# Optimization experiments

Measured on AMD Instinct MI355X. Metric: run time of the kernel, lower is better.

The kernel has to match this reference:

```python
import jax, jax.numpy as jnp
import numpy as np

NPOINT = 2048  # N // stride


def sqdist(a, b):
    # a: [B,M,3], b: [B,N,3] -> squared euclidean distances [B,M,N] (== cdist(...)**2)
    return (jnp.sum(a * a, -1)[:, :, None] + jnp.sum(b * b, -1)[:, None, :]
            - 2.0 * jnp.einsum('bmc,bnc->bmn', a, b))


def farthest_point_sample(xyz, npoint):
    # xyz [B,N,3] -> int32 [B,npoint]; deterministic start at point 0
    B, N, _ = xyz.shape

    def step(carry, _):
        distance, farthest = carry
        centroid = jnp.take_along_axis(xyz, farthest[:, None, None], axis=1)  # [B,1,3]
        d = jnp.sum((xyz - centroid) ** 2, -1)                                # [B,N]
        distance = jnp.minimum(distance, d)
        nxt = jnp.argmax(distance, -1).astype(jnp.int32)
        return (distance, nxt), farthest

    init = (jnp.full((B, N), 1e10, xyz.dtype), jnp.zeros((B,), jnp.int32))
    _, idx = jax.lax.scan(step, init, None, length=npoint)
    return idx.T  # [B, npoint]


def ball_query(radius, k, xyz, new_xyz):
    # faithful to torch ball_query: mask out-of-radius as N, sort indices, take first k,
    # replace padding with the first valid neighbor
    B, N, _ = xyz.shape
    sqd = sqdist(new_xyz, xyz)                                   # [B,S,N]
    gi = jnp.where(sqd > radius ** 2, N, jnp.arange(N, dtype=jnp.int32))
    gi = jnp.sort(gi, axis=-1)[:, :, :k]                         # [B,S,k]
    first = gi[:, :, :1]
    return jnp.where(gi == N, first, gi)


def three_interpolation(points, features, query):
    # points [B,S,3], features [B,D,S], query [B,N,3] -> [B,D,N]
    d = sqdist(query, points)                                    # [B,N,S]
    neg, idx = jax.lax.top_k(-d, 3)                              # 3 smallest dists
    w = 1.0 / (-neg + 1e-8)
    w = w / jnp.sum(w, -1, keepdims=True)                        # [B,N,3]
    g = jnp.take_along_axis(features[:, :, None, :], idx[:, None, :, :], axis=3)  # [B,D,N,3]
    return jnp.sum(g * w[:, None, :, :], -1)


def setup_inputs() -> dict:
    key = jax.random.key(0)
    k1, k2, k3, k4 = jax.random.split(key, 4)
    xyz = jax.random.uniform(k1, (4, 8192, 3), dtype=jnp.float32)
    features = jax.random.normal(k2, (4, 64, 8192), dtype=jnp.float32)
    W1 = jax.random.normal(k3, (128, 67), dtype=jnp.float32) * 0.05   # (3+64)->128 pointwise conv
    W2 = jax.random.normal(k4, (128, 192), dtype=jnp.float32) * 0.05  # (64+128)->128 pointwise conv
    return {"xyz": xyz, "features": features, "W1": W1, "W2": W2}


def reference(xyz, features, W1, W2):
    RADIUS, K = 0.2, 16
    # --- set abstraction (SABlock): FPS -> ball query -> group -> conv -> maxpool ---
    sidx = farthest_point_sample(xyz, NPOINT)                        # [B,S]
    new_xyz = jnp.take_along_axis(xyz, sidx[:, :, None], axis=1)     # [B,S,3]
    nidx = ball_query(RADIUS, K, xyz, new_xyz)                       # [B,S,K]
    gxyz = jnp.take_along_axis(xyz[:, None, :, :], nidx[:, :, :, None], axis=2)  # [B,S,K,3]
    rel = gxyz - new_xyz[:, :, None, :]                              # relative coords
    gfeat = jnp.take_along_axis(features[:, :, None, :], nidx[:, None, :, :], axis=3)  # [B,D,S,K]
    grouped = jnp.concatenate([rel.transpose(0, 3, 1, 2), gfeat], axis=1)  # [B,3+D,S,K]
    h = jax.nn.relu(jnp.einsum('od,bdsk->bosk', W1, grouped))
    sub_x = jnp.max(h, -1)                                           # [B,O,S]
    # --- feature propagation (UpBlock): 3-NN interpolation back to N -> concat -> conv ---
    lerp = three_interpolation(new_xyz, sub_x, xyz)                  # [B,O,N]
    cat = jnp.concatenate([features, lerp], axis=1)                  # [B,D+O,N]
    return jax.nn.relu(jnp.einsum('od,bdn->bon', W2, cat))           # [B,O,N]
```

## Files before the change

### kernel.cpp

```cpp
#include <hip/hip_runtime.h>
#include <hip/hip_bf16.h>

#define BATCH 4
#define NPTS  8192
#define NSAMP 2048
#define NK    16
#define CFEAT 64
#define CG    67
#define CO1   128
#define CCAT  192
#define CO2   128

#define DEV __device__ __forceinline__

typedef float f32x2 __attribute__((ext_vector_type(2)));

DEV float n3(float x, float y, float z) {
    return __fadd_rn(__fadd_rn(__fmul_rn(x, x), __fmul_rn(y, y)), __fmul_rn(z, z));
}
DEV float dot3(float ax, float ay, float az, float bx, float by, float bz) {
    return __fmaf_rn(az, bz, __fmaf_rn(ay, by, __fmul_rn(ax, bx)));
}
DEV float sqd_expand(float an, float bn, float d) {
    return __fsub_rn(__fadd_rn(an, bn), __fmul_rn(2.0f, d));
}

DEV f32x2 pk_add(f32x2 a, f32x2 b) {
    f32x2 d;
    asm("v_pk_add_f32 %0, %1, %2" : "=v"(d) : "v"(a), "v"(b));
    return d;
}
DEV f32x2 pk_mul(f32x2 a, f32x2 b) {
    f32x2 d;
    asm("v_pk_mul_f32 %0, %1, %2" : "=v"(d) : "v"(a), "v"(b));
    return d;
}

#define DPPMAX(x, ctrl)                                                        \
    x = fmaxf(x, __int_as_float(__builtin_amdgcn_update_dpp(                   \
            __float_as_int(x), __float_as_int(x), (ctrl), 0xF, 0xF, false)))

template <int CTRL>
DEV void dpp_shr_max64(unsigned& hi, unsigned& lo) {
    unsigned nh = (unsigned)__builtin_amdgcn_update_dpp((int)hi, (int)hi, CTRL, 0xF, 0xF, false);
    unsigned nl = (unsigned)__builtin_amdgcn_update_dpp((int)lo, (int)lo, CTRL, 0xF, 0xF, false);
    unsigned long long a = ((unsigned long long)hi << 32) | lo;
    unsigned long long n = ((unsigned long long)nh << 32) | nl;
    if (n > a) { hi = nh; lo = nl; }
}

DEV float rlane(float v, int l) {
    return __int_as_float(__builtin_amdgcn_readlane(__float_as_int(v), l));
}

__global__ __launch_bounds__(256) void transpose_kernel(const float* __restrict__ F,
                                                        float* __restrict__ T) {
    __shared__ float tile[64][65];
    const int b = blockIdx.y;
    const int n0 = blockIdx.x * 64;
    const int tx = threadIdx.x & 63, ty = threadIdx.x >> 6;
    const float* Fb = F + (size_t)b * CFEAT * NPTS;
    float* Tb = T + (size_t)b * NPTS * CFEAT;
#pragma unroll
    for (int i = 0; i < 16; i++) {
        int c = ty + i * 4;
        tile[c][tx] = Fb[(size_t)c * NPTS + n0 + tx];
    }
    __syncthreads();
#pragma unroll
    for (int i = 0; i < 16; i++) {
        int r = ty + i * 4;
        Tb[(size_t)(n0 + r) * CFEAT + tx] = tile[tx][r];
    }
}

__global__ __launch_bounds__(512, 2) void fps_kernel(const float* __restrict__ xyz,
                                                     float* __restrict__ new_xyz) {
    const int b = blockIdx.x;
    const int t = threadIdx.x;
    const int lane = t & 63, wv = t >> 6;
    const float* X = xyz + (size_t)b * NPTS * 3;

    __shared__ f32x2 sxy[NPTS];
    __shared__ float szl[NPTS];
    __shared__ unsigned long long wred[2][8];

    f32x2 px[8], py[8], pz[8], dd[8];
    {
        const float4* X4 = (const float4*)X;
#pragma unroll
        for (int g = 0; g < 4; g++) {
            float4 f0 = X4[t * 12 + g * 3 + 0];
            float4 f1 = X4[t * 12 + g * 3 + 1];
            float4 f2 = X4[t * 12 + g * 3 + 2];
            px[2*g+0].x = f0.x; py[2*g+0].x = f0.y; pz[2*g+0].x = f0.z;
            px[2*g+0].y = f0.w; py[2*g+0].y = f1.x; pz[2*g+0].y = f1.y;
            px[2*g+1].x = f1.z; py[2*g+1].x = f1.w; pz[2*g+1].x = f2.x;
            px[2*g+1].y = f2.y; py[2*g+1].y = f2.z; pz[2*g+1].y = f2.w;
        }
#pragma unroll
        for (int j = 0; j < 8; j++) {
            int p = t * 16 + 2 * j;
            sxy[p].x = px[j].x; sxy[p].y = py[j].x; szl[p] = pz[j].x;
            sxy[p+1].x = px[j].y; sxy[p+1].y = py[j].y; szl[p+1] = pz[j].y;
            dd[j].x = 1e10f; dd[j].y = 1e10f;
        }
    }
    __syncthreads();

    f32x2 c0 = sxy[0];
    float cx = c0.x, cy = c0.y, cz = szl[0];
    if (t == 0) {
        size_t o = (size_t)b * NSAMP * 3;
        new_xyz[o + 0] = cx; new_xyz[o + 1] = cy; new_xyz[o + 2] = cz;
    }

    int par = 0;
    for (int s = 1; s < NSAMP; s++) {
        const float ncx = -cx, ncy = -cy, ncz = -cz;
        const f32x2 vcx = {ncx, ncx}, vcy = {ncy, ncy}, vcz = {ncz, ncz};
#pragma unroll
        for (int j = 0; j < 8; j++) {
            f32x2 dx = pk_add(px[j], vcx);
            f32x2 dy = pk_add(py[j], vcy);
            f32x2 dz = pk_add(pz[j], vcz);
            f32x2 d = pk_add(pk_add(pk_mul(dx, dx), pk_mul(dy, dy)), pk_mul(dz, dz));
            dd[j].x = fminf(dd[j].x, d.x);
            dd[j].y = fminf(dd[j].y, d.y);
        }
        float m[8];
#pragma unroll
        for (int j = 0; j < 8; j++) m[j] = fmaxf(dd[j].x, dd[j].y);
#pragma unroll
        for (int j = 0; j < 4; j++) m[j] = fmaxf(m[j], m[j + 4]);
        float bv = fmaxf(fmaxf(m[0], m[1]), fmaxf(m[2], m[3]));
        int bj = 15;
#pragma unroll
        for (int j = 14; j >= 0; --j) {
            float dj = (j & 1) ? dd[j >> 1].y : dd[j >> 1].x;
            if (dj == bv) bj = j;
        }
        const int lidx = t * 16 + bj;

        float wm = bv;
        DPPMAX(wm, 0x111);
        DPPMAX(wm, 0x112);
        DPPMAX(wm, 0x114);
        DPPMAX(wm, 0x118);
        DPPMAX(wm, 0x142);
        DPPMAX(wm, 0x143);
        const float wmax = __int_as_float(
            __builtin_amdgcn_readlane(__float_as_int(wm), 63));
        const unsigned long long em = __ballot(bv == wmax);
        const int wl = (int)__builtin_ctzll(em);
        const int widx = __builtin_amdgcn_readlane(lidx, wl);

        if (lane == 0)
            wred[par][wv] = ((unsigned long long)__float_as_uint(wmax) << 32)
                          | (unsigned int)(~widx);
        __syncthreads();

        unsigned long long v = wred[par][lane & 7];
        unsigned hi = (unsigned)(v >> 32), lo = (unsigned)v;
        dpp_shr_max64<0x111>(hi, lo);
        dpp_shr_max64<0x112>(hi, lo);
        dpp_shr_max64<0x114>(hi, lo);
        const int idx = ~__builtin_amdgcn_readlane((int)lo, 7);

        f32x2 cxy = sxy[idx];
        cz = szl[idx];
        cx = cxy.x; cy = cxy.y;
        if (t == 0) {
            size_t o = ((size_t)b * NSAMP + s) * 3;
            new_xyz[o + 0] = cx; new_xyz[o + 1] = cy; new_xyz[o + 2] = cz;
        }
        par ^= 1;
    }
}

__global__ __launch_bounds__(256) void ballq_kernel(const float* __restrict__ xyz,
                                                    const float* __restrict__ new_xyz,
                                                    int* __restrict__ nidx) {
    const int wv = threadIdx.x >> 6, lane = threadIdx.x & 63;
    const int q = blockIdx.x * 4 + wv;
    const int b = q >> 11;
    const float* X = xyz + (size_t)b * NPTS * 3;
    const float* Q = new_xyz + (size_t)q * 3;
    const float qx = Q[0], qy = Q[1], qz = Q[2];
    const float an = n3(qx, qy, qz);

    __shared__ int nb[4][NK];
    int cnt = 0;
    for (int base = 0; base < NPTS && cnt < NK; base += 64) {
        int p = base + lane;
        float x = X[p * 3 + 0], y = X[p * 3 + 1], z = X[p * 3 + 2];
        float bn = n3(x, y, z);
        float dt = dot3(qx, qy, qz, x, y, z);
        float sq = sqd_expand(an, bn, dt);
        bool in = (sq <= 0.04f);
        unsigned long long m = __ballot(in);
        if (in) {
            int pos = cnt + (int)__popcll(m & ((1ull << lane) - 1ull));
            if (pos < NK) nb[wv][pos] = p;
        }
        cnt += (int)__popcll(m);
    }
    __syncthreads();
    if (lane < NK) {
        int c = cnt < NK ? cnt : NK;
        int v = (lane < c) ? nb[wv][lane] : nb[wv][0];
        nidx[(size_t)q * NK + lane] = v;
    }
}

__global__ __launch_bounds__(256) void group_mlp_kernel(const float* __restrict__ xyz,
                                                        const float* __restrict__ featT,
                                                        const float* __restrict__ new_xyz,
                                                        const int* __restrict__ nidx,
                                                        const float* __restrict__ W1,
                                                        float* __restrict__ subxT) {
    __shared__ f32x2 w1t2[CG][64];
    for (int i = threadIdx.x; i < CG * 64; i += 256) {
        int d = i >> 6, o = i & 63;
        w1t2[d][o].x = W1[(size_t)o * CG + d];
        w1t2[d][o].y = W1[(size_t)(o + 64) * CG + d];
    }
    __syncthreads();
    const int lane = threadIdx.x & 63, wv = threadIdx.x >> 6;

    for (int q = blockIdx.x * 4 + wv; q < BATCH * NSAMP; q += gridDim.x * 4) {
        const int b = q >> 11;
        const float* Q = new_xyz + (size_t)q * 3;
        const float qx = Q[0], qy = Q[1], qz = Q[2];
        const int* NB = nidx + (size_t)q * NK;
        float m0 = 0.0f, m1 = 0.0f;
#pragma unroll 1
        for (int k = 0; k < NK; k += 2) {
            const int n0 = NB[k], n1 = NB[k + 1];
            const float* P0 = xyz + ((size_t)b * NPTS + n0) * 3;
            const float* P1 = xyz + ((size_t)b * NPTS + n1) * 3;
            float rx0 = P0[0] - qx, ry0 = P0[1] - qy, rz0 = P0[2] - qz;
            float rx1 = P1[0] - qx, ry1 = P1[1] - qy, rz1 = P1[2] - qz;
            float fv0 = featT[((size_t)b * NPTS + n0) * CFEAT + lane];
            float fv1 = featT[((size_t)b * NPTS + n1) * CFEAT + lane];
            f32x2 w0 = w1t2[0][lane], w1 = w1t2[1][lane], w2 = w1t2[2][lane];
            float a0 = fmaf(w0.x, rx0, fmaf(w1.x, ry0, w2.x * rz0));
            float a1 = fmaf(w0.y, rx0, fmaf(w1.y, ry0, w2.y * rz0));
            float c0 = fmaf(w0.x, rx1, fmaf(w1.x, ry1, w2.x * rz1));
            float c1 = fmaf(w0.y, rx1, fmaf(w1.y, ry1, w2.y * rz1));
#pragma unroll
            for (int c = 0; c < 64; c++) {
                f32x2 w = w1t2[3 + c][lane];
                float g0 = rlane(fv0, c);
                float g1 = rlane(fv1, c);
                a0 = fmaf(w.x, g0, a0);
                a1 = fmaf(w.y, g0, a1);
                c0 = fmaf(w.x, g1, c0);
                c1 = fmaf(w.y, g1, c1);
            }
            m0 = fmaxf(m0, fmaxf(a0, c0));
            m1 = fmaxf(m1, fmaxf(a1, c1));
        }
        subxT[(size_t)q * CO1 + lane] = m0;
        subxT[(size_t)q * CO1 + 64 + lane] = m1;
    }
}

DEV void ins3(float dd, int jj,
              float& d0, int& i0, float& d1, int& i1, float& d2, int& i2) {
    bool c2 = (dd < d2) || (dd == d2 && jj < i2);
    if (c2) { d2 = dd; i2 = jj; }
    bool c1 = (d2 < d1) || (d2 == d1 && i2 < i1);
    if (c1) { float tv = d1; int ti = i1; d1 = d2; i1 = i2; d2 = tv; i2 = ti; }
    bool c0 = (d1 < d0) || (d1 == d0 && i1 < i0);
    if (c0) { float tv = d0; int ti = i0; d0 = d1; i0 = i1; d1 = tv; i1 = ti; }
}

__global__ __launch_bounds__(256) void interp_w2_kernel(const float* __restrict__ xyz,
                                                        const float* __restrict__ new_xyz,
                                                        const float* __restrict__ featT,
                                                        const float* __restrict__ subxT,
                                                        const float* __restrict__ W2,
                                                        float* __restrict__ out) {
    __shared__ f32x2 w2t2[CCAT][64];
    for (int i = threadIdx.x; i < CCAT * 64; i += 256) {
        int d = i >> 6, o = i & 63;
        w2t2[d][o].x = W2[(size_t)o * CCAT + d];
        w2t2[d][o].y = W2[(size_t)(o + 64) * CCAT + d];
    }
    __syncthreads();
    const int lane = threadIdx.x & 63, wv = threadIdx.x >> 6;

    for (int q = blockIdx.x * 4 + wv; q < BATCH * NPTS; q += gridDim.x * 4) {
        const int b = q >> 13, n = q & (NPTS - 1);
        const float* P = xyz + (size_t)q * 3;
        const float qx = P[0], qy = P[1], qz = P[2];
        const float an = n3(qx, qy, qz);

        float d0 = 1e30f, d1 = 1e30f, d2 = 1e30f;
        int i0 = 0x7fffffff, i1 = 0x7fffffff, i2 = 0x7fffffff;
        for (int j = lane; j < NSAMP; j += 64) {
            const float* C = new_xyz + ((size_t)b * NSAMP + j) * 3;
            float x = C[0], y = C[1], z = C[2];
            float bn = n3(x, y, z);
            float dt = dot3(qx, qy, qz, x, y, z);
            float dd = sqd_expand(an, bn, dt);
            ins3(dd, j, d0, i0, d1, i1, d2, i2);
        }
#pragma unroll
        for (int off = 32; off > 0; off >>= 1) {
            float e0 = __shfl_xor(d0, off); int f0 = __shfl_xor(i0, off);
            float e1 = __shfl_xor(d1, off); int f1 = __shfl_xor(i1, off);
            float e2 = __shfl_xor(d2, off); int f2 = __shfl_xor(i2, off);
            ins3(e0, f0, d0, i0, d1, i1, d2, i2);
            ins3(e1, f1, d0, i0, d1, i1, d2, i2);
            ins3(e2, f2, d0, i0, d1, i1, d2, i2);
        }
        float w0 = 1.0f / (d0 + 1e-8f);
        float w1 = 1.0f / (d1 + 1e-8f);
        float w2 = 1.0f / (d2 + 1e-8f);
        float sw = (w0 + w1) + w2;
        w0 /= sw; w1 /= sw; w2 /= sw;

        const float* S = subxT + (size_t)b * NSAMP * CO1;
        float L0 = S[(size_t)i0 * CO1 + lane] * w0
                 + S[(size_t)i1 * CO1 + lane] * w1
                 + S[(size_t)i2 * CO1 + lane] * w2;
        float L1 = S[(size_t)i0 * CO1 + 64 + lane] * w0
                 + S[(size_t)i1 * CO1 + 64 + lane] * w1
                 + S[(size_t)i2 * CO1 + 64 + lane] * w2;

        float fv = featT[((size_t)b * NPTS + n) * CFEAT + lane];

        float a0 = 0.0f, a1 = 0.0f;
#pragma unroll
        for (int c = 0; c < 64; c++) {
            f32x2 w = w2t2[c][lane];
            float g = rlane(fv, c);
            a0 = fmaf(w.x, g, a0); a1 = fmaf(w.y, g, a1);
        }
#pragma unroll
        for (int c = 0; c < 64; c++) {
            f32x2 w = w2t2[64 + c][lane];
            float g = rlane(L0, c);
            a0 = fmaf(w.x, g, a0); a1 = fmaf(w.y, g, a1);
        }
#pragma unroll
        for (int c = 0; c < 64; c++) {
            f32x2 w = w2t2[128 + c][lane];
            float g = rlane(L1, c);
            a0 = fmaf(w.x, g, a0); a1 = fmaf(w.y, g, a1);
        }
        out[((size_t)b * CO2 + lane) * NPTS + n] = fmaxf(a0, 0.0f);
        out[((size_t)b * CO2 + 64 + lane) * NPTS + n] = fmaxf(a1, 0.0f);
    }
}

extern "C" void kernel_launch(void* const* d_in, const int* in_sizes, int n_in,
                              void* d_out, int out_size, void* d_ws, size_t ws_size,
                              hipStream_t stream) {
    const float* xyz      = (const float*)d_in[0];
    const float* features = (const float*)d_in[1];
    const float* W1       = (const float*)d_in[2];
    const float* W2       = (const float*)d_in[3];
    float* out = (float*)d_out;

    float* featT   = (float*)d_ws;
    float* new_xyz = featT + (size_t)BATCH * NPTS * CFEAT;
    int*   nidx    = (int*)(new_xyz + (size_t)BATCH * NSAMP * 3);
    float* subxT   = (float*)(nidx + (size_t)BATCH * NSAMP * NK);

    transpose_kernel<<<dim3(NPTS / 64, BATCH), 256, 0, stream>>>(features, featT);
    fps_kernel<<<BATCH, 512, 0, stream>>>(xyz, new_xyz);
    ballq_kernel<<<(BATCH * NSAMP) / 4, 256, 0, stream>>>(xyz, new_xyz, nidx);
    group_mlp_kernel<<<512, 256, 0, stream>>>(xyz, featT, new_xyz, nidx, W1, subxT);
    interp_w2_kernel<<<256, 256, 0, stream>>>(xyz, new_xyz, featT, subxT, W2, out);
}
```

Baseline: 2.512 ms.

## Morton-sort FPS points per wave and skip waves outside new centroid's reach

FPS now runs with 1024 threads per batch. Points are bucketed by a coarse Morton key using a shared-memory counting sort, so each wave holds a spatially compact cluster. Each wave keeps a bounding sphere and its current max min-distance, and skips the distance update and reduction when the new centroid cannot reduce any of its distances. The in-wave argmax tie-break now uses original point indices via a second DPP max, so results stay deterministic. The interp kernel moves to 512-thread blocks. The risk is added setup cost, plus divergence if most waves still fall inside the threshold.

```diff
diff --git a/kernel.cpp b/kernel.cpp
--- a/kernel.cpp
+++ b/kernel.cpp
@@ -40,6 +40,13 @@
     x = fmaxf(x, __int_as_float(__builtin_amdgcn_update_dpp(                   \
             __float_as_int(x), __float_as_int(x), (ctrl), 0xF, 0xF, false)))
 
+#define DPPMAXU(x, ctrl)                                                       \
+    do {                                                                       \
+        unsigned _o = (unsigned)__builtin_amdgcn_update_dpp(                   \
+            (int)(x), (int)(x), (ctrl), 0xF, 0xF, false);                      \
+        x = (x > _o) ? x : _o;                                                 \
+    } while (0)
+
 template <int CTRL>
 DEV void dpp_shr_max64(unsigned& hi, unsigned& lo) {
     unsigned nh = (unsigned)__builtin_amdgcn_update_dpp((int)hi, (int)hi, CTRL, 0xF, 0xF, false);
@@ -51,6 +58,16 @@
 
 DEV float rlane(float v, int l) {
     return __int_as_float(__builtin_amdgcn_readlane(__float_as_int(v), l));
+}
+
+DEV int mortkey(float x, float y, float z) {
+    int ix = min(7, (int)(x * 8.0f));
+    int iy = min(7, (int)(y * 8.0f));
+    int iz = min(7, (int)(z * 8.0f));
+    int oct = ((iz >> 2) << 2) | ((iy >> 2) << 1) | (ix >> 2);
+    int m = (ix & 1) | ((iy & 1) << 1) | ((iz & 1) << 2)
+          | (((ix >> 1) & 1) << 3) | (((iy >> 1) & 1) << 4) | (((iz >> 1) & 1) << 5);
+    return (oct << 6) | m;
 }
 
 __global__ __launch_bounds__(256) void transpose_kernel(const float* __restrict__ F,
@@ -74,8 +91,8 @@
     }
 }
 
-__global__ __launch_bounds__(512, 2) void fps_kernel(const float* __restrict__ xyz,
-                                                     float* __restrict__ new_xyz) {
+__global__ __launch_bounds__(1024, 4) void fps_kernel(const float* __restrict__ xyz,
+                                                      float* __restrict__ new_xyz) {
     const int b = blockIdx.x;
     const int t = threadIdx.x;
     const int lane = t & 63, wv = t >> 6;
@@ -83,30 +100,98 @@
 
     __shared__ f32x2 sxy[NPTS];
     __shared__ float szl[NPTS];
-    __shared__ unsigned long long wred[2][8];
-
-    f32x2 px[8], py[8], pz[8], dd[8];
+    __shared__ unsigned short sidx[NPTS];
+    __shared__ unsigned int cnt_off[512];
+    __shared__ unsigned long long wred[2][16];
+
     {
         const float4* X4 = (const float4*)X;
-#pragma unroll
-        for (int g = 0; g < 4; g++) {
-            float4 f0 = X4[t * 12 + g * 3 + 0];
-            float4 f1 = X4[t * 12 + g * 3 + 1];
-            float4 f2 = X4[t * 12 + g * 3 + 2];
-            px[2*g+0].x = f0.x; py[2*g+0].x = f0.y; pz[2*g+0].x = f0.z;
-            px[2*g+0].y = f0.w; py[2*g+0].y = f1.x; pz[2*g+0].y = f1.y;
-            px[2*g+1].x = f1.z; py[2*g+1].x = f1.w; pz[2*g+1].x = f2.x;
-            px[2*g+1].y = f2.y; py[2*g+1].y = f2.z; pz[2*g+1].y = f2.w;
-        }
+        float4 f0 = X4[t*6+0], f1 = X4[t*6+1], f2 = X4[t*6+2];
+        float4 f3 = X4[t*6+3], f4 = X4[t*6+4], f5 = X4[t*6+5];
+        float ox[8], oy[8], oz[8];
+        ox[0]=f0.x; oy[0]=f0.y; oz[0]=f0.z;
+        ox[1]=f0.w; oy[1]=f1.x; oz[1]=f1.y;
+        ox[2]=f1.z; oy[2]=f1.w; oz[2]=f2.x;
+        ox[3]=f2.y; oy[3]=f2.z; oz[3]=f2.w;
+        ox[4]=f3.x; oy[4]=f3.y; oz[4]=f3.z;
+        ox[5]=f3.w; oy[5]=f4.x; oz[5]=f4.y;
+        ox[6]=f4.z; oy[6]=f4.w; oz[6]=f5.x;
+        ox[7]=f5.y; oy[7]=f5.z; oz[7]=f5.w;
 #pragma unroll
         for (int j = 0; j < 8; j++) {
-            int p = t * 16 + 2 * j;
-            sxy[p].x = px[j].x; sxy[p].y = py[j].x; szl[p] = pz[j].x;
-            sxy[p+1].x = px[j].y; sxy[p+1].y = py[j].y; szl[p+1] = pz[j].y;
-            dd[j].x = 1e10f; dd[j].y = 1e10f;
+            int p = t * 8 + j;
+            sxy[p].x = ox[j]; sxy[p].y = oy[j]; szl[p] = oz[j];
+        }
+        if (t < 512) cnt_off[t] = 0;
+        __syncthreads();
+#pragma unroll
+        for (int j = 0; j < 8; j++)
+            atomicAdd(&cnt_off[mortkey(ox[j], oy[j], oz[j])], 1u);
+        __syncthreads();
+        if (t < 64) {
+            unsigned h[8], lsum = 0;
+#pragma unroll
+            for (int k = 0; k < 8; k++) { h[k] = cnt_off[t * 8 + k]; lsum += h[k]; }
+            unsigned run = lsum;
+#pragma unroll
+            for (int d = 1; d < 64; d <<= 1) {
+                unsigned o = __shfl_up(run, d);
+                if (lane >= d) run += o;
+            }
+            unsigned acc = run - lsum;
+#pragma unroll
+            for (int k = 0; k < 8; k++) { cnt_off[t * 8 + k] = acc; acc += h[k]; }
+        }
+        __syncthreads();
+#pragma unroll
+        for (int j = 0; j < 8; j++) {
+            int key = mortkey(ox[j], oy[j], oz[j]);
+            unsigned pos = atomicAdd(&cnt_off[key], 1u);
+            sidx[pos] = (unsigned short)(t * 8 + j);
         }
     }
     __syncthreads();
+
+    f32x2 px[4], py[4], pz[4], dd[4];
+    int pid[8];
+#pragma unroll
+    for (int j = 0; j < 8; j++) {
+        int p = sidx[t * 8 + j];
+        pid[j] = p;
+        f32x2 xy = sxy[p];
+        float z = szl[p];
+        if (j & 1) { px[j >> 1].y = xy.x; py[j >> 1].y = xy.y; pz[j >> 1].y = z; }
+        else       { px[j >> 1].x = xy.x; py[j >> 1].x = xy.y; pz[j >> 1].x = z; }
+    }
+#pragma unroll
+    for (int j = 0; j < 4; j++) { dd[j].x = 1e10f; dd[j].y = 1e10f; }
+
+    float mnx = 1e30f, mxx = -1e30f, mny = 1e30f, mxy = -1e30f, mnz = 1e30f, mxz = -1e30f;
+#pragma unroll
+    for (int j = 0; j < 4; j++) {
+        mnx = fminf(mnx, fminf(px[j].x, px[j].y)); mxx = fmaxf(mxx, fmaxf(px[j].x, px[j].y));
+        mny = fminf(mny, fminf(py[j].x, py[j].y)); mxy = fmaxf(mxy, fmaxf(py[j].x, py[j].y));
+        mnz = fminf(mnz, fminf(pz[j].x, pz[j].y)); mxz = fmaxf(mxz, fmaxf(pz[j].x, pz[j].y));
+    }
+#pragma unroll
+    for (int off = 32; off > 0; off >>= 1) {
+        mnx = fminf(mnx, __shfl_xor(mnx, off)); mxx = fmaxf(mxx, __shfl_xor(mxx, off));
+        mny = fminf(mny, __shfl_xor(mny, off)); mxy = fmaxf(mxy, __shfl_xor(mxy, off));
+        mnz = fminf(mnz, __shfl_xor(mnz, off)); mxz = fmaxf(mxz, __shfl_xor(mxz, off));
+    }
+    const float rx = 0.5f * (mnx + mxx), ry = 0.5f * (mny + mxy), rz = 0.5f * (mnz + mxz);
+    float r2m = 0.0f;
+#pragma unroll
+    for (int j = 0; j < 4; j++) {
+        float ax = px[j].x - rx, ay = py[j].x - ry, az = pz[j].x - rz;
+        float bx2 = px[j].y - rx, by2 = py[j].y - ry, bz2 = pz[j].y - rz;
+        r2m = fmaxf(r2m, ax * ax + ay * ay + az * az);
+        r2m = fmaxf(r2m, bx2 * bx2 + by2 * by2 + bz2 * bz2);
+    }
+#pragma unroll
+    for (int off = 32; off > 0; off >>= 1)
+        r2m = fmaxf(r2m, __shfl_xor(r2m, off));
+    const float rad = sqrtf(r2m) * 1.0001f + 1e-6f;
 
     f32x2 c0 = sxy[0];
     float cx = c0.x, cy = c0.y, cz = szl[0];
@@ -115,57 +200,56 @@
         new_xyz[o + 0] = cx; new_xyz[o + 1] = cy; new_xyz[o + 2] = cz;
     }
 
+    unsigned long long wpack = 0;
+    float sb = 1e19f;
+
     int par = 0;
     for (int s = 1; s < NSAMP; s++) {
-        const float ncx = -cx, ncy = -cy, ncz = -cz;
-        const f32x2 vcx = {ncx, ncx}, vcy = {ncy, ncy}, vcz = {ncz, ncz};
-#pragma unroll
-        for (int j = 0; j < 8; j++) {
-            f32x2 dx = pk_add(px[j], vcx);
-            f32x2 dy = pk_add(py[j], vcy);
-            f32x2 dz = pk_add(pz[j], vcz);
-            f32x2 d = pk_add(pk_add(pk_mul(dx, dx), pk_mul(dy, dy)), pk_mul(dz, dz));
-            dd[j].x = fminf(dd[j].x, d.x);
-            dd[j].y = fminf(dd[j].y, d.y);
-        }
-        float m[8];
-#pragma unroll
-        for (int j = 0; j < 8; j++) m[j] = fmaxf(dd[j].x, dd[j].y);
-#pragma unroll
-        for (int j = 0; j < 4; j++) m[j] = fmaxf(m[j], m[j + 4]);
-        float bv = fmaxf(fmaxf(m[0], m[1]), fmaxf(m[2], m[3]));
-        int bj = 15;
-#pragma unroll
-        for (int j = 14; j >= 0; --j) {
-            float dj = (j & 1) ? dd[j >> 1].y : dd[j >> 1].x;
-            if (dj == bv) bj = j;
-        }
-        const int lidx = t * 16 + bj;
-
-        float wm = bv;
-        DPPMAX(wm, 0x111);
-        DPPMAX(wm, 0x112);
-        DPPMAX(wm, 0x114);
-        DPPMAX(wm, 0x118);
-        DPPMAX(wm, 0x142);
-        DPPMAX(wm, 0x143);
-        const float wmax = __int_as_float(
-            __builtin_amdgcn_readlane(__float_as_int(wm), 63));
-        const unsigned long long em = __ballot(bv == wmax);
-        const int wl = (int)__builtin_ctzll(em);
-        const int widx = __builtin_amdgcn_readlane(lidx, wl);
-
-        if (lane == 0)
-            wred[par][wv] = ((unsigned long long)__float_as_uint(wmax) << 32)
-                          | (unsigned int)(~widx);
+        float ddx = cx - rx, ddy = cy - ry, ddz = cz - rz;
+        float dc2 = ddx * ddx + ddy * ddy + ddz * ddz;
+        float thr = rad + sb;
+        if (dc2 < thr * thr) {
+            const float ncx = -cx, ncy = -cy, ncz = -cz;
+            const f32x2 vcx = {ncx, ncx}, vcy = {ncy, ncy}, vcz = {ncz, ncz};
+#pragma unroll
+            for (int j = 0; j < 4; j++) {
+                f32x2 dx = pk_add(px[j], vcx);
+                f32x2 dy = pk_add(py[j], vcy);
+                f32x2 dz = pk_add(pz[j], vcz);
+                f32x2 d = pk_add(pk_add(pk_mul(dx, dx), pk_mul(dy, dy)), pk_mul(dz, dz));
+                dd[j].x = fminf(dd[j].x, d.x);
+                dd[j].y = fminf(dd[j].y, d.y);
+            }
+            float m0 = fmaxf(dd[0].x, dd[0].y), m1 = fmaxf(dd[1].x, dd[1].y);
+            float m2 = fmaxf(dd[2].x, dd[2].y), m3 = fmaxf(dd[3].x, dd[3].y);
+            float bv = fmaxf(fmaxf(m0, m1), fmaxf(m2, m3));
+            int nb = 0x7fffffff;
+#pragma unroll
+            for (int j = 0; j < 8; j++) {
+                float dj = (j & 1) ? dd[j >> 1].y : dd[j >> 1].x;
+                if (dj == bv) nb = min(nb, pid[j]);
+            }
+            float wm = bv;
+            DPPMAX(wm, 0x111); DPPMAX(wm, 0x112); DPPMAX(wm, 0x114);
+            DPPMAX(wm, 0x118); DPPMAX(wm, 0x142); DPPMAX(wm, 0x143);
+            const float wmax = rlane(wm, 63);
+            unsigned tv = (bv == wmax) ? (unsigned)(~nb) : 0u;
+            DPPMAXU(tv, 0x111); DPPMAXU(tv, 0x112); DPPMAXU(tv, 0x114);
+            DPPMAXU(tv, 0x118); DPPMAXU(tv, 0x142); DPPMAXU(tv, 0x143);
+            const unsigned tmax = (unsigned)__builtin_amdgcn_readlane((int)tv, 63);
+            wpack = ((unsigned long long)__float_as_uint(wmax) << 32) | tmax;
+            sb = sqrtf(wmax) * 1.0001f + 1e-6f;
+        }
+        if (lane == 0) wred[par][wv] = wpack;
         __syncthreads();
 
-        unsigned long long v = wred[par][lane & 7];
+        unsigned long long v = wred[par][lane & 15];
         unsigned hi = (unsigned)(v >> 32), lo = (unsigned)v;
         dpp_shr_max64<0x111>(hi, lo);
         dpp_shr_max64<0x112>(hi, lo);
         dpp_shr_max64<0x114>(hi, lo);
-        const int idx = ~__builtin_amdgcn_readlane((int)lo, 7);
+        dpp_shr_max64<0x118>(hi, lo);
+        const int idx = ~__builtin_amdgcn_readlane((int)lo, 15);
 
         f32x2 cxy = sxy[idx];
         cz = szl[idx];
@@ -276,14 +360,14 @@
     if (c0) { float tv = d0; int ti = i0; d0 = d1; i0 = i1; d1 = tv; i1 = ti; }
 }
 
-__global__ __launch_bounds__(256) void interp_w2_kernel(const float* __restrict__ xyz,
+__global__ __launch_bounds__(512) void interp_w2_kernel(const float* __restrict__ xyz,
                                                         const float* __restrict__ new_xyz,
                                                         const float* __restrict__ featT,
                                                         const float* __restrict__ subxT,
                                                         const float* __restrict__ W2,
                                                         float* __restrict__ out) {
     __shared__ f32x2 w2t2[CCAT][64];
-    for (int i = threadIdx.x; i < CCAT * 64; i += 256) {
+    for (int i = threadIdx.x; i < CCAT * 64; i += 512) {
         int d = i >> 6, o = i & 63;
         w2t2[d][o].x = W2[(size_t)o * CCAT + d];
         w2t2[d][o].y = W2[(size_t)(o + 64) * CCAT + d];
@@ -291,7 +375,7 @@
     __syncthreads();
     const int lane = threadIdx.x & 63, wv = threadIdx.x >> 6;
 
-    for (int q = blockIdx.x * 4 + wv; q < BATCH * NPTS; q += gridDim.x * 4) {
+    for (int q = blockIdx.x * 8 + wv; q < BATCH * NPTS; q += gridDim.x * 8) {
         const int b = q >> 13, n = q & (NPTS - 1);
         const float* P = xyz + (size_t)q * 3;
         const float qx = P[0], qy = P[1], qz = P[2];
@@ -371,8 +455,8 @@
     float* subxT   = (float*)(nidx + (size_t)BATCH * NSAMP * NK);
 
     transpose_kernel<<<dim3(NPTS / 64, BATCH), 256, 0, stream>>>(features, featT);
-    fps_kernel<<<BATCH, 512, 0, stream>>>(xyz, new_xyz);
+    fps_kernel<<<BATCH, 1024, 0, stream>>>(xyz, new_xyz);
     ballq_kernel<<<(BATCH * NSAMP) / 4, 256, 0, stream>>>(xyz, new_xyz, nidx);
     group_mlp_kernel<<<512, 256, 0, stream>>>(xyz, featT, new_xyz, nidx, W1, subxT);
-    interp_w2_kernel<<<256, 256, 0, stream>>>(xyz, new_xyz, featT, subxT, W2, out);
-}
+    interp_w2_kernel<<<256, 512, 0, stream>>>(xyz, new_xyz, featT, subxT, W2, out);
+}
```

Result: slower. 3.096 ms (+23.3%).
